# Kernel tuning notes

Measured on AMD Instinct MI355X. Metric: run time of the kernel, lower is better.

The kernel has to match this reference:

```python
import jax, jax.numpy as jnp
import numpy as np

B, C, H, W = 16, 64, 64, 64
C1, C2 = 8, 32  # block_channels_1 = C/8, block_channels_2 = C/2


def _conv1x1(x, w, b):
    # x: [B,C,H,W], w: [O,C] (1x1 kernel), b: [O]
    return jnp.einsum('bchw,oc->bohw', x, w) + b[None, :, None, None]


def _maxpool2(x):
    # MaxPool2d(kernel_size=2): window 2x2, stride 2, no padding
    return jax.lax.reduce_window(x, -jnp.inf, jax.lax.max,
                                 (1, 1, 2, 2), (1, 1, 2, 2), 'VALID')


def setup_inputs() -> dict:
    key = jax.random.key(0)
    ks = jax.random.split(key, 10)
    s = lambda fan_in: 1.0 / np.sqrt(fan_in)
    return {
        'nonlocal_input': jax.random.normal(ks[0], (B, C, H, W), jnp.float32),
        # spectral-normalized conv weights are treated as the effective (already
        # normalized) weights; 1x1 kernels stored as [out, in]
        'w_delta': jax.random.normal(ks[1], (C1, C), jnp.float32) * s(C),
        'b_delta': jax.random.normal(ks[2], (C1,), jnp.float32) * 0.01,
        'w_phi': jax.random.normal(ks[3], (C1, C), jnp.float32) * s(C),
        'b_phi': jax.random.normal(ks[4], (C1,), jnp.float32) * 0.01,
        'w_g': jax.random.normal(ks[5], (C2, C), jnp.float32) * s(C),
        'b_g': jax.random.normal(ks[6], (C2,), jnp.float32) * 0.01,
        'w_last': jax.random.normal(ks[7], (C, C2), jnp.float32) * s(C2),
        'b_last': jax.random.normal(ks[8], (C,), jnp.float32) * 0.01,
        # torch init is zeros; use a nonzero value so the attention path matters
        'gamma': jnp.asarray([0.7], jnp.float32),
    }


def reference(nonlocal_input, w_delta, b_delta, w_phi, b_phi, w_g, b_g,
              w_last, b_last, gamma):
    x = nonlocal_input
    b, c, h, w = x.shape

    # delta: [B,C1,H,W] -> [B, HW, C1]
    delta = _conv1x1(x, w_delta, b_delta)
    delta = jnp.transpose(delta, (0, 2, 3, 1)).reshape(b, h * w, C1)

    # phi: conv + pool -> [B,C1,H/2,W/2]; NOTE: the original permutes
    # (1,0,2,3) BEFORE reshaping to [B, C1, HW/4] (faithful to source).
    phi = _maxpool2(_conv1x1(x, w_phi, b_phi))
    phi = jnp.transpose(phi, (1, 0, 2, 3)).reshape(b, C1, -1)

    # attention: [B, HW, HW/4]
    attn = jax.nn.softmax(jnp.einsum('bnk,bkm->bnm', delta, phi), axis=-1)

    # g: conv + pool -> [B, HW/4, C2]
    g = _maxpool2(_conv1x1(x, w_g, b_g))
    g = jnp.transpose(g, (0, 2, 3, 1)).reshape(b, -1, C2)

    out = jnp.einsum('bnm,bmc->bnc', attn, g)          # [B, HW, C2]
    out = out.reshape(b, h, w, C2).transpose(0, 3, 1, 2)  # [B, C2, H, W]

    return gamma[0] * _conv1x1(out, w_last, b_last) + x
```

## Files before the change

### kernel.cpp

```cpp
#include <hip/hip_runtime.h>
#include <hip/hip_bf16.h>
#include <math.h>

typedef __attribute__((ext_vector_type(8))) short bf16x8;
typedef __attribute__((ext_vector_type(4))) float f32x4;

#define B_   16
#define C_   64
#define C1_  8
#define C2_  32
#define HW_  4096
#define M_   1024
#define LOG2E 1.4426950408889634f
#define MFMA_BF16 __builtin_amdgcn_mfma_f32_16x16x32_bf16

__device__ __forceinline__ unsigned short f2bf(float f) {
  union { float f; unsigned u; } v; v.f = f;
  unsigned r = (v.u + 0x7fffu + ((v.u >> 16) & 1u)) >> 16;
  return (unsigned short)r;
}
__device__ __forceinline__ float bf2f(unsigned short h) {
  union { unsigned u; float f; } v; v.u = ((unsigned)h) << 16;
  return v.f;
}

__global__ __launch_bounds__(256, 4)
void k_pre(const float* __restrict__ x,
           const float* __restrict__ w_delta, const float* __restrict__ b_delta,
           const float* __restrict__ w_phi, const float* __restrict__ b_phi,
           const float* __restrict__ w_g,   const float* __restrict__ b_g,
           unsigned short* __restrict__ delta_s,
           unsigned short* __restrict__ phi_s,
           unsigned short* __restrict__ g_t) {
  __shared__ float comb[2*64*49];
  int tid = threadIdx.x;

  int qt  = tid >> 6;
  int sub = tid & 63;
  int id  = blockIdx.x * 64 + sub;
  int pix = id & 3;
  int pm  = id >> 2;
  int b = pm >> 10;
  int m = pm & 1023;
  int py = 2*(m >> 5) + (pix >> 1);
  int px = 2*(m & 31) + (pix & 1);
  int n = py * 64 + px;

  int c0 = __builtin_amdgcn_readfirstlane(qt << 4);

  const float* xp = x + ((size_t)b*C_ + c0)*HW_ + n;
  float xv[16];
  #pragma unroll
  for (int i = 0; i < 16; ++i) xv[i] = xp[(size_t)i * HW_];

  float ad[8], ap[8], ag[32];
  #pragma unroll
  for (int o = 0; o < 8; ++o) {
    const float* wd = w_delta + o*C_ + c0;
    float a = 0.f;
    #pragma unroll
    for (int i = 0; i < 16; ++i) a += xv[i]*wd[i];
    ad[o] = a;
  }
  #pragma unroll
  for (int o = 0; o < 8; ++o) {
    const float* wp = w_phi + o*C_ + c0;
    float a = 0.f;
    #pragma unroll
    for (int i = 0; i < 16; ++i) a += xv[i]*wp[i];
    ap[o] = a;
  }
  #pragma unroll
  for (int o = 0; o < 32; ++o) {
    const float* wg = w_g + o*C_ + c0;
    float a = 0.f;
    #pragma unroll
    for (int i = 0; i < 16; ++i) a += xv[i]*wg[i];
    ag[o] = a;
  }

  if (qt == 1 || qt == 3) {
    float* cb = comb + (((qt >> 1)*64) + sub)*49;
    #pragma unroll
    for (int o = 0; o < 8; ++o) cb[o] = ad[o];
    #pragma unroll
    for (int o = 0; o < 8; ++o) cb[8+o] = ap[o];
    #pragma unroll
    for (int o = 0; o < 32; ++o) cb[16+o] = ag[o];
  }
  __syncthreads();
  if (qt == 0 || qt == 2) {
    const float* cb = comb + (((qt >> 1)*64) + sub)*49;
    #pragma unroll
    for (int o = 0; o < 8; ++o) ad[o] += cb[o];
    #pragma unroll
    for (int o = 0; o < 8; ++o) ap[o] += cb[8+o];
    #pragma unroll
    for (int o = 0; o < 32; ++o) ag[o] += cb[16+o];
  }
  __syncthreads();
  if (qt == 2) {
    float* cb = comb + sub*49;
    #pragma unroll
    for (int o = 0; o < 8; ++o) cb[o] = ad[o];
    #pragma unroll
    for (int o = 0; o < 8; ++o) cb[8+o] = ap[o];
    #pragma unroll
    for (int o = 0; o < 32; ++o) cb[16+o] = ag[o];
  }
  __syncthreads();
  if (qt == 0) {
    const float* cb = comb + sub*49;
    #pragma unroll
    for (int o = 0; o < 8; ++o) ad[o] += cb[o];
    #pragma unroll
    for (int o = 0; o < 8; ++o) ap[o] += cb[8+o];
    #pragma unroll
    for (int o = 0; o < 32; ++o) ag[o] += cb[16+o];

    {
      union { unsigned short s[8]; uint4 v; } dh, dl;
      #pragma unroll
      for (int o = 0; o < 8; ++o) {
        float v = (ad[o] + b_delta[o]) * LOG2E;
        unsigned short hi = f2bf(v);
        dh.s[o] = hi;
        dl.s[o] = f2bf(v - bf2f(hi));
      }
      uint4* dp = (uint4*)(delta_s + ((size_t)b*HW_ + n)*16);
      dp[0] = dh.v;
      dp[1] = dl.v;
    }

    #pragma unroll
    for (int o = 0; o < 8; ++o) {
      float v = ap[o];
      v = fmaxf(v, __shfl_xor(v, 1));
      v = fmaxf(v, __shfl_xor(v, 2));
      ap[o] = v;
    }
    #pragma unroll
    for (int o = 0; o < 32; ++o) {
      float v = ag[o];
      v = fmaxf(v, __shfl_xor(v, 1));
      v = fmaxf(v, __shfl_xor(v, 2));
      ag[o] = v;
    }

    if ((sub & 3) == 0) {
      #pragma unroll
      for (int cp = 0; cp < 8; ++cp) {
        int f = cp*16 + b;
        float v = ap[cp] + b_phi[cp];
        unsigned short hi = f2bf(v);
        unsigned short* pr = phi_s + ((size_t)(f >> 3)*M_ + m)*16;
        pr[f & 7]       = hi;
        pr[8 + (f & 7)] = f2bf(v - bf2f(hi));
      }
      #pragma unroll
      for (int o = 0; o < 32; ++o)
        g_t[((size_t)b*C2_ + o)*M_ + m] = f2bf(ag[o] + b_g[o]);
    }
  }
}

__global__ __launch_bounds__(512, 4)
void k_attn(const float* __restrict__ x,
            const unsigned short* __restrict__ delta_s,
            const unsigned short* __restrict__ phi_s,
            const unsigned short* __restrict__ g_t,
            const float* __restrict__ w_last,
            const float* __restrict__ b_last,
            const float* __restrict__ gamma,
            float* __restrict__ out) {
  __shared__ __align__(16) unsigned char lds_raw[50176];
  unsigned short* phi_lds = (unsigned short*)lds_raw;
  unsigned short* g_lds   = (unsigned short*)(lds_raw + 16384);
  float* o_sh = (float*)lds_raw;
  float* cmb  = (float*)(lds_raw + 16896);

  int tid  = threadIdx.x;
  int lane = tid & 63;
  int wv   = tid >> 6;
  int rg   = wv & 3;
  int kh   = wv >> 2;
  int r    = lane & 15;
  int q    = lane >> 4;
  int bx = blockIdx.x;
  int b  = bx >> 5;
  int n0 = (bx & 31) * 128;

  bf16x8 df[2];
  {
    const unsigned short* dp =
        delta_s + ((size_t)b*HW_ + n0 + rg*32 + r)*16 + (q & 1)*8;
    df[0] = *(const bf16x8*)(dp);
    df[1] = *(const bf16x8*)(dp + 16*16);
  }

  int phi_off = (q >> 1) * 8;
  int key0 = (r >> 2)*8 + (r & 3);
  int key1 = key0 + 4;

  bf16x8 ones;
  #pragma unroll
  for (int i = 0; i < 8; ++i) ones[i] = (short)0x3F80;

  f32x4 acc[2][2];
  f32x4 den[2];
  f32x4 zero = {0,0,0,0};
  #pragma unroll
  for (int t = 0; t < 2; ++t) { acc[t][0] = zero; acc[t][1] = zero; den[t] = zero; }

  for (int p = 0; p < 2; ++p) {
    if (p) __syncthreads();
    {
      const uint4* psrc = (const uint4*)(phi_s + ((size_t)b*M_ + p*512)*16);
      uint4* pdst = (uint4*)phi_lds;
      #pragma unroll
      for (int u = 0; u < 2; ++u) pdst[tid + u*512] = psrc[tid + u*512];
      #pragma unroll
      for (int u = 0; u < 4; ++u) {
        int uu = tid + u*512;
        int c2 = uu >> 6, pos = uu & 63;
        *(uint4*)(g_lds + c2*520 + pos*8) =
            *(const uint4*)(g_t + ((size_t)b*C2_ + c2)*M_ + p*512 + pos*8);
      }
    }
    __syncthreads();

    #pragma unroll 2
    for (int kc = 0; kc < 256; kc += 32) {
      int kl = kh*256 + kc;
      bf16x8 aphi0 = *(const bf16x8*)(phi_lds + (size_t)(kl + key0)*16 + phi_off);
      bf16x8 aphi1 = *(const bf16x8*)(phi_lds + (size_t)(kl + key1)*16 + phi_off);
      bf16x8 bg0   = *(const bf16x8*)(g_lds + r*520        + kl + q*8);
      bf16x8 bg1   = *(const bf16x8*)(g_lds + (16 + r)*520 + kl + q*8);

      #pragma unroll
      for (int t = 0; t < 2; ++t) {
        f32x4 s0 = MFMA_BF16(aphi0, df[t], zero, 0, 0, 0);
        f32x4 s1 = MFMA_BF16(aphi1, df[t], zero, 0, 0, 0);
        union { bf16x8 v; __hip_bfloat162 h[4]; } e;
        e.h[0] = __float22bfloat162_rn(make_float2(__builtin_amdgcn_exp2f(s0[0]),
                                                   __builtin_amdgcn_exp2f(s0[1])));
        e.h[1] = __float22bfloat162_rn(make_float2(__builtin_amdgcn_exp2f(s0[2]),
                                                   __builtin_amdgcn_exp2f(s0[3])));
        e.h[2] = __float22bfloat162_rn(make_float2(__builtin_amdgcn_exp2f(s1[0]),
                                                   __builtin_amdgcn_exp2f(s1[1])));
        e.h[3] = __float22bfloat162_rn(make_float2(__builtin_amdgcn_exp2f(s1[2]),
                                                   __builtin_amdgcn_exp2f(s1[3])));
        acc[t][0] = MFMA_BF16(e.v, bg0, acc[t][0], 0, 0, 0);
        acc[t][1] = MFMA_BF16(e.v, bg1, acc[t][1], 0, 0, 0);
        den[t]    = MFMA_BF16(e.v, ones, den[t], 0, 0, 0);
      }
    }
  }

  __syncthreads();
  if (kh == 1) {
    #pragma unroll
    for (int t = 0; t < 2; ++t) {
      #pragma unroll
      for (int reg = 0; reg < 4; ++reg) {
        int row = rg*32 + t*16 + q*4 + reg;
        cmb[row*34 + r]      = acc[t][0][reg];
        cmb[row*34 + 16 + r] = acc[t][1][reg];
        if (r == 0) cmb[row*34 + 32] = den[t][reg];
      }
    }
  }
  __syncthreads();
  if (kh == 0) {
    #pragma unroll
    for (int t = 0; t < 2; ++t) {
      #pragma unroll
      for (int reg = 0; reg < 4; ++reg) {
        int row = rg*32 + t*16 + q*4 + reg;
        float o0 = acc[t][0][reg] + cmb[row*34 + r];
        float o1 = acc[t][1][reg] + cmb[row*34 + 16 + r];
        float dn = den[t][reg]    + cmb[row*34 + 32];
        float iv = __builtin_amdgcn_rcpf(dn);
        o_sh[row*33 + r]      = o0 * iv;
        o_sh[row*33 + 16 + r] = o1 * iv;
      }
    }
  }
  __syncthreads();

  int rr  = tid & 127;
  int wqu = __builtin_amdgcn_readfirstlane(tid >> 7);
  float o_reg[32];
  #pragma unroll
  for (int c = 0; c < 32; ++c) o_reg[c] = o_sh[rr*33 + c];
  float gm = gamma[0];
  for (int i = 0; i < 16; ++i) {
    int co = wqu*16 + i;
    const float* wl = w_last + co*32;
    float a = b_last[co];
    #pragma unroll
    for (int c = 0; c < 32; ++c) a += wl[c] * o_reg[c];
    size_t oi = ((size_t)b*C_ + co)*HW_ + (size_t)(n0 + rr);
    out[oi] = gm * a + x[oi];
  }
}

extern "C" void kernel_launch(void* const* d_in, const int* in_sizes, int n_in,
                              void* d_out, int out_size, void* d_ws, size_t ws_size,
                              hipStream_t stream) {
  const float* x       = (const float*)d_in[0];
  const float* w_delta = (const float*)d_in[1];
  const float* b_delta = (const float*)d_in[2];
  const float* w_phi   = (const float*)d_in[3];
  const float* b_phi   = (const float*)d_in[4];
  const float* w_g     = (const float*)d_in[5];
  const float* b_g     = (const float*)d_in[6];
  const float* w_last  = (const float*)d_in[7];
  const float* b_last  = (const float*)d_in[8];
  const float* gamma   = (const float*)d_in[9];
  float* out = (float*)d_out;

  unsigned short* ws = (unsigned short*)d_ws;
  unsigned short* phi_s   = ws;
  unsigned short* g_t     = ws + (size_t)B_*M_*16;
  unsigned short* delta_s = ws + (size_t)B_*M_*16 + (size_t)B_*C2_*M_;

  hipLaunchKernelGGL(k_pre, dim3(1024), dim3(256), 0, stream,
                     x, w_delta, b_delta, w_phi, b_phi, w_g, b_g,
                     delta_s, phi_s, g_t);
  hipLaunchKernelGGL(k_attn, dim3(512), dim3(512), 0, stream,
                     x, delta_s, phi_s, g_t, w_last, b_last, gamma, out);
}
```

Baseline: 112.9 us.

## Split attention keys four ways per block with 64-row wave tiles

Reorganizes k_attn wave mapping from 4 row-groups x 2 key halves to 2 row-groups x 4 key quarters, so each wave handles 64 query rows and reuses each loaded phi/g fragment across four MFMA tiles. This halves LDS fragment loads per MFMA but needs a three-buffer cross-wave reduction, larger LDS footprint, and more accumulator registers, which may hurt occupancy under launch_bounds(512,4).

```diff
diff --git a/kernel.cpp b/kernel.cpp
--- a/kernel.cpp
+++ b/kernel.cpp
@@ -173,29 +173,31 @@
             const float* __restrict__ b_last,
             const float* __restrict__ gamma,
             float* __restrict__ out) {
-  __shared__ __align__(16) unsigned char lds_raw[50176];
+  __shared__ __align__(16) unsigned char lds_raw[52224];
   unsigned short* phi_lds = (unsigned short*)lds_raw;
   unsigned short* g_lds   = (unsigned short*)(lds_raw + 16384);
-  float* o_sh = (float*)lds_raw;
-  float* cmb  = (float*)(lds_raw + 16896);
+  float* cmb0 = (float*)lds_raw;
+  float* cmb1 = (float*)(lds_raw + 17408);
+  float* cmb2 = (float*)(lds_raw + 34816);
 
   int tid  = threadIdx.x;
   int lane = tid & 63;
   int wv   = tid >> 6;
-  int rg   = wv & 3;
-  int kh   = wv >> 2;
+  int rg   = wv & 1;
+  int kh   = wv >> 1;
   int r    = lane & 15;
   int q    = lane >> 4;
   int bx = blockIdx.x;
   int b  = bx >> 5;
   int n0 = (bx & 31) * 128;
 
-  bf16x8 df[2];
+  bf16x8 df[4];
   {
     const unsigned short* dp =
-        delta_s + ((size_t)b*HW_ + n0 + rg*32 + r)*16 + (q & 1)*8;
-    df[0] = *(const bf16x8*)(dp);
-    df[1] = *(const bf16x8*)(dp + 16*16);
+        delta_s + ((size_t)b*HW_ + n0 + rg*64 + r)*16 + (q & 1)*8;
+    #pragma unroll
+    for (int t = 0; t < 4; ++t)
+      df[t] = *(const bf16x8*)(dp + t*16*16);
   }
 
   int phi_off = (q >> 1) * 8;
@@ -206,11 +208,11 @@
   #pragma unroll
   for (int i = 0; i < 8; ++i) ones[i] = (short)0x3F80;
 
-  f32x4 acc[2][2];
-  f32x4 den[2];
+  f32x4 acc[4][2];
+  f32x4 den[4];
   f32x4 zero = {0,0,0,0};
   #pragma unroll
-  for (int t = 0; t < 2; ++t) { acc[t][0] = zero; acc[t][1] = zero; den[t] = zero; }
+  for (int t = 0; t < 4; ++t) { acc[t][0] = zero; acc[t][1] = zero; den[t] = zero; }
 
   for (int p = 0; p < 2; ++p) {
     if (p) __syncthreads();
@@ -230,15 +232,15 @@
     __syncthreads();
 
     #pragma unroll 2
-    for (int kc = 0; kc < 256; kc += 32) {
-      int kl = kh*256 + kc;
+    for (int kc = 0; kc < 128; kc += 32) {
+      int kl = kh*128 + kc;
       bf16x8 aphi0 = *(const bf16x8*)(phi_lds + (size_t)(kl + key0)*16 + phi_off);
       bf16x8 aphi1 = *(const bf16x8*)(phi_lds + (size_t)(kl + key1)*16 + phi_off);
       bf16x8 bg0   = *(const bf16x8*)(g_lds + r*520        + kl + q*8);
       bf16x8 bg1   = *(const bf16x8*)(g_lds + (16 + r)*520 + kl + q*8);
 
       #pragma unroll
-      for (int t = 0; t < 2; ++t) {
+      for (int t = 0; t < 4; ++t) {
         f32x4 s0 = MFMA_BF16(aphi0, df[t], zero, 0, 0, 0);
         f32x4 s1 = MFMA_BF16(aphi1, df[t], zero, 0, 0, 0);
         union { bf16x8 v; __hip_bfloat162 h[4]; } e;
@@ -258,31 +260,35 @@
   }
 
   __syncthreads();
-  if (kh == 1) {
-    #pragma unroll
-    for (int t = 0; t < 2; ++t) {
+  if (kh != 0) {
+    float* cb = (kh == 1) ? cmb0 : (kh == 2) ? cmb1 : cmb2;
+    #pragma unroll
+    for (int t = 0; t < 4; ++t) {
       #pragma unroll
       for (int reg = 0; reg < 4; ++reg) {
-        int row = rg*32 + t*16 + q*4 + reg;
-        cmb[row*34 + r]      = acc[t][0][reg];
-        cmb[row*34 + 16 + r] = acc[t][1][reg];
-        if (r == 0) cmb[row*34 + 32] = den[t][reg];
+        int row = rg*64 + t*16 + q*4 + reg;
+        cb[row*34 + r]      = acc[t][0][reg];
+        cb[row*34 + 16 + r] = acc[t][1][reg];
+        if (r == 0) cb[row*34 + 32] = den[t][reg];
       }
     }
   }
   __syncthreads();
   if (kh == 0) {
     #pragma unroll
-    for (int t = 0; t < 2; ++t) {
+    for (int t = 0; t < 4; ++t) {
       #pragma unroll
       for (int reg = 0; reg < 4; ++reg) {
-        int row = rg*32 + t*16 + q*4 + reg;
-        float o0 = acc[t][0][reg] + cmb[row*34 + r];
-        float o1 = acc[t][1][reg] + cmb[row*34 + 16 + r];
-        float dn = den[t][reg]    + cmb[row*34 + 32];
+        int row = rg*64 + t*16 + q*4 + reg;
+        float o0 = acc[t][0][reg] + cmb0[row*34 + r]
+                 + cmb1[row*34 + r] + cmb2[row*34 + r];
+        float o1 = acc[t][1][reg] + cmb0[row*34 + 16 + r]
+                 + cmb1[row*34 + 16 + r] + cmb2[row*34 + 16 + r];
+        float dn = den[t][reg] + cmb0[row*34 + 32]
+                 + cmb1[row*34 + 32] + cmb2[row*34 + 32];
         float iv = __builtin_amdgcn_rcpf(dn);
-        o_sh[row*33 + r]      = o0 * iv;
-        o_sh[row*33 + 16 + r] = o1 * iv;
+        cmb0[row*34 + r]      = o0 * iv;
+        cmb0[row*34 + 16 + r] = o1 * iv;
       }
     }
   }
@@ -292,7 +298,7 @@
   int wqu = __builtin_amdgcn_readfirstlane(tid >> 7);
   float o_reg[32];
   #pragma unroll
-  for (int c = 0; c < 32; ++c) o_reg[c] = o_sh[rr*33 + c];
+  for (int c = 0; c < 32; ++c) o_reg[c] = cmb0[rr*34 + c];
   float gm = gamma[0];
   for (int i = 0; i < 16; ++i) {
     int co = wqu*16 + i;
```

After: 114.6 us. About the same (+1.5%).

## Fold w_last projection into pooled g before attention, widen PV to 64 channels

Applied to the files above, without the earlier changes.

Uses linearity to apply the final 1x1 conv (w_last) to the pooled g values in the pre-pass, which is valid because softmax rows sum to one. The attention kernel then accumulates directly into 64 output channels and only adds bias, gamma and the residual. This drops the per-pixel 32x64 epilogue GEMV in k_attn. In exchange the PV MFMA work doubles, the g tensor doubles in size, and the key loop is split into four smaller LDS stages, with an XOR swizzle added to avoid LDS bank conflicts.

```diff
diff --git a/kernel.cpp b/kernel.cpp
--- a/kernel.cpp
+++ b/kernel.cpp
@@ -29,11 +29,19 @@
            const float* __restrict__ w_delta, const float* __restrict__ b_delta,
            const float* __restrict__ w_phi, const float* __restrict__ b_phi,
            const float* __restrict__ w_g,   const float* __restrict__ b_g,
+           const float* __restrict__ w_last,
            unsigned short* __restrict__ delta_s,
            unsigned short* __restrict__ phi_s,
-           unsigned short* __restrict__ g_t) {
+           unsigned short* __restrict__ g2_t) {
   __shared__ float comb[2*64*49];
+  __shared__ float wlds[64*33];
   int tid = threadIdx.x;
+
+  #pragma unroll
+  for (int k = 0; k < 8; ++k) {
+    int e = tid + k*256;
+    wlds[(e >> 5)*33 + (e & 31)] = w_last[e];
+  }
 
   int qt  = tid >> 6;
   int sub = tid & 63;
@@ -157,9 +165,30 @@
         pr[f & 7]       = hi;
         pr[8 + (f & 7)] = f2bf(v - bf2f(hi));
       }
-      #pragma unroll
-      for (int o = 0; o < 32; ++o)
-        g_t[((size_t)b*C2_ + o)*M_ + m] = f2bf(ag[o] + b_g[o]);
+      int mi = sub >> 2;
+      float* al = comb + mi*33;
+      #pragma unroll
+      for (int o = 0; o < 32; ++o) al[o] = ag[o] + b_g[o];
+    }
+  }
+  __syncthreads();
+
+  {
+    int mi  = tid & 15;
+    int cow = tid >> 4;
+    int bb  = blockIdx.x >> 6;
+    int mb  = (blockIdx.x & 63) * 16;
+    float av[32];
+    #pragma unroll
+    for (int c = 0; c < 32; ++c) av[c] = comb[mi*33 + c];
+    #pragma unroll
+    for (int j = 0; j < 4; ++j) {
+      int co = cow + j*16;
+      const float* wl = wlds + co*33;
+      float a = 0.f;
+      #pragma unroll
+      for (int c = 0; c < 32; ++c) a += av[c] * wl[c];
+      g2_t[((size_t)bb*64 + co)*M_ + mb + mi] = f2bf(a);
     }
   }
 }
@@ -168,16 +197,14 @@
 void k_attn(const float* __restrict__ x,
             const unsigned short* __restrict__ delta_s,
             const unsigned short* __restrict__ phi_s,
-            const unsigned short* __restrict__ g_t,
-            const float* __restrict__ w_last,
+            const unsigned short* __restrict__ g2_t,
             const float* __restrict__ b_last,
             const float* __restrict__ gamma,
             float* __restrict__ out) {
-  __shared__ __align__(16) unsigned char lds_raw[50176];
+  __shared__ __align__(16) unsigned char lds_raw[40960];
   unsigned short* phi_lds = (unsigned short*)lds_raw;
-  unsigned short* g_lds   = (unsigned short*)(lds_raw + 16384);
-  float* o_sh = (float*)lds_raw;
-  float* cmb  = (float*)(lds_raw + 16896);
+  unsigned char*  g2_lds  = lds_raw + 8192;
+  float* cmb = (float*)lds_raw;
 
   int tid  = threadIdx.x;
   int lane = tid & 63;
@@ -206,36 +233,44 @@
   #pragma unroll
   for (int i = 0; i < 8; ++i) ones[i] = (short)0x3F80;
 
-  f32x4 acc[2][2];
+  f32x4 acc[2][4];
   f32x4 den[2];
   f32x4 zero = {0,0,0,0};
   #pragma unroll
-  for (int t = 0; t < 2; ++t) { acc[t][0] = zero; acc[t][1] = zero; den[t] = zero; }
-
-  for (int p = 0; p < 2; ++p) {
+  for (int t = 0; t < 2; ++t) {
+    #pragma unroll
+    for (int cg = 0; cg < 4; ++cg) acc[t][cg] = zero;
+    den[t] = zero;
+  }
+
+  for (int p = 0; p < 4; ++p) {
     if (p) __syncthreads();
     {
-      const uint4* psrc = (const uint4*)(phi_s + ((size_t)b*M_ + p*512)*16);
-      uint4* pdst = (uint4*)phi_lds;
-      #pragma unroll
-      for (int u = 0; u < 2; ++u) pdst[tid + u*512] = psrc[tid + u*512];
-      #pragma unroll
-      for (int u = 0; u < 4; ++u) {
-        int uu = tid + u*512;
-        int c2 = uu >> 6, pos = uu & 63;
-        *(uint4*)(g_lds + c2*520 + pos*8) =
-            *(const uint4*)(g_t + ((size_t)b*C2_ + c2)*M_ + p*512 + pos*8);
+      const uint4* psrc = (const uint4*)(phi_s + ((size_t)b*M_ + p*256)*16);
+      ((uint4*)phi_lds)[tid] = psrc[tid];
+      #pragma unroll
+      for (int i = 0; i < 4; ++i) {
+        int u = tid + i*512;
+        int co = u >> 5, pos = u & 31;
+        unsigned byte = (unsigned)(co*512 + pos*16) ^ (unsigned)((co & 7) << 4);
+        *(uint4*)(g2_lds + byte) =
+            *(const uint4*)(g2_t + ((size_t)b*64 + co)*M_ + p*256 + pos*8);
       }
     }
     __syncthreads();
 
     #pragma unroll 2
-    for (int kc = 0; kc < 256; kc += 32) {
-      int kl = kh*256 + kc;
+    for (int kc = 0; kc < 128; kc += 32) {
+      int kl = kh*128 + kc;
       bf16x8 aphi0 = *(const bf16x8*)(phi_lds + (size_t)(kl + key0)*16 + phi_off);
       bf16x8 aphi1 = *(const bf16x8*)(phi_lds + (size_t)(kl + key1)*16 + phi_off);
-      bf16x8 bg0   = *(const bf16x8*)(g_lds + r*520        + kl + q*8);
-      bf16x8 bg1   = *(const bf16x8*)(g_lds + (16 + r)*520 + kl + q*8);
+      bf16x8 bg[4];
+      #pragma unroll
+      for (int cg = 0; cg < 4; ++cg) {
+        unsigned byte = (unsigned)((cg*16 + r)*512 + kl*2 + q*16)
+                      ^ (unsigned)((r & 7) << 4);
+        bg[cg] = *(const bf16x8*)(g2_lds + byte);
+      }
 
       #pragma unroll
       for (int t = 0; t < 2; ++t) {
@@ -250,9 +285,10 @@
                                                    __builtin_amdgcn_exp2f(s1[1])));
         e.h[3] = __float22bfloat162_rn(make_float2(__builtin_amdgcn_exp2f(s1[2]),
                                                    __builtin_amdgcn_exp2f(s1[3])));
-        acc[t][0] = MFMA_BF16(e.v, bg0, acc[t][0], 0, 0, 0);
-        acc[t][1] = MFMA_BF16(e.v, bg1, acc[t][1], 0, 0, 0);
-        den[t]    = MFMA_BF16(e.v, ones, den[t], 0, 0, 0);
+        #pragma unroll
+        for (int cg = 0; cg < 4; ++cg)
+          acc[t][cg] = MFMA_BF16(e.v, bg[cg], acc[t][cg], 0, 0, 0);
+        den[t] = MFMA_BF16(e.v, ones, den[t], 0, 0, 0);
       }
     }
   }
@@ -264,9 +300,10 @@
       #pragma unroll
       for (int reg = 0; reg < 4; ++reg) {
         int row = rg*32 + t*16 + q*4 + reg;
-        cmb[row*34 + r]      = acc[t][0][reg];
-        cmb[row*34 + 16 + r] = acc[t][1][reg];
-        if (r == 0) cmb[row*34 + 32] = den[t][reg];
+        #pragma unroll
+        for (int cg = 0; cg < 4; ++cg)
+          cmb[row*66 + cg*16 + r] = acc[t][cg][reg];
+        if (r == 0) cmb[row*66 + 64] = den[t][reg];
       }
     }
   }
@@ -277,12 +314,13 @@
       #pragma unroll
       for (int reg = 0; reg < 4; ++reg) {
         int row = rg*32 + t*16 + q*4 + reg;
-        float o0 = acc[t][0][reg] + cmb[row*34 + r];
-        float o1 = acc[t][1][reg] + cmb[row*34 + 16 + r];
-        float dn = den[t][reg]    + cmb[row*34 + 32];
+        float dn = den[t][reg] + cmb[row*66 + 64];
         float iv = __builtin_amdgcn_rcpf(dn);
-        o_sh[row*33 + r]      = o0 * iv;
-        o_sh[row*33 + 16 + r] = o1 * iv;
+        #pragma unroll
+        for (int cg = 0; cg < 4; ++cg) {
+          float o = acc[t][cg][reg] + cmb[row*66 + cg*16 + r];
+          cmb[row*66 + cg*16 + r] = o * iv;
+        }
       }
     }
   }
@@ -290,18 +328,13 @@
 
   int rr  = tid & 127;
   int wqu = __builtin_amdgcn_readfirstlane(tid >> 7);
-  float o_reg[32];
-  #pragma unroll
-  for (int c = 0; c < 32; ++c) o_reg[c] = o_sh[rr*33 + c];
   float gm = gamma[0];
+  #pragma unroll
   for (int i = 0; i < 16; ++i) {
     int co = wqu*16 + i;
-    const float* wl = w_last + co*32;
-    float a = b_last[co];
-    #pragma unroll
-    for (int c = 0; c < 32; ++c) a += wl[c] * o_reg[c];
+    float val = cmb[rr*66 + co];
     size_t oi = ((size_t)b*C_ + co)*HW_ + (size_t)(n0 + rr);
-    out[oi] = gm * a + x[oi];
+    out[oi] = gm * (val + b_last[co]) + x[oi];
   }
 }
 
@@ -322,12 +355,12 @@
 
   unsigned short* ws = (unsigned short*)d_ws;
   unsigned short* phi_s   = ws;
-  unsigned short* g_t     = ws + (size_t)B_*M_*16;
-  unsigned short* delta_s = ws + (size_t)B_*M_*16 + (size_t)B_*C2_*M_;
+  unsigned short* g2_t    = ws + (size_t)B_*M_*16;
+  unsigned short* delta_s = ws + (size_t)B_*M_*16 + (size_t)B_*64*M_;
 
   hipLaunchKernelGGL(k_pre, dim3(1024), dim3(256), 0, stream,
-                     x, w_delta, b_delta, w_phi, b_phi, w_g, b_g,
-                     delta_s, phi_s, g_t);
+                     x, w_delta, b_delta, w_phi, b_phi, w_g, b_g, w_last,
+                     delta_s, phi_s, g2_t);
   hipLaunchKernelGGL(k_attn, dim3(512), dim3(512), 0, stream,
-                     x, delta_s, phi_s, g_t, w_last, b_last, gamma, out);
-}
+                     x, delta_s, phi_s, g2_t, b_last, gamma, out);
+}
```

After: 116.4 us. 1.03x slower.
